# Performance work log

Hardware: AMD Instinct MI355X
Metric: run time of the kernel (lower is better)

The kernel has to match this reference:

```python
import jax, jax.numpy as jnp
import numpy as np

B, N, C, O = 8, 4096, 256, 256  # batch, nodes, in_channels, out_channels
DENSITY = 0.01


def _cheb_k2(x_flat, A, W0, W1, b):
    """PyG ChebConv with K=2, sym normalization, lambda_max=2.
    Scaled Laplacian reduces to Lhat = -D^{-1/2} A D^{-1/2} (self-loops removed,
    diagonal of I - Ahat cancels with the fill_value=-1 self loops).
    Only the first N flattened nodes have edges (faithful to the source bug)."""
    n = A.shape[0]
    A = A * (1.0 - jnp.eye(n, dtype=A.dtype))  # remove_self_loops
    deg = A.sum(axis=1)                         # scatter(edge_weight, row)
    dis = jnp.where(deg > 0, jax.lax.rsqrt(jnp.where(deg > 0, deg, 1.0)), 0.0)
    Ahat = (dis[:, None] * A) * dis[None, :]    # D^{-1/2} A D^{-1/2}
    out = x_flat @ W0                           # Tx_0 term, all B*N nodes
    prop = -(Ahat @ x_flat[:n])                 # Tx_1 = Lhat x, first N nodes only
    out = out.at[:n].add(prop @ W1)
    return out + b


def setup_inputs() -> dict:
    key = jax.random.key(0)
    ks = jax.random.split(key, 12)
    x = jax.random.normal(ks[0], (B, N, C), jnp.float32)

    def adj(k):
        u = jax.random.uniform(k, (N, N), jnp.float32)
        return jnp.where(u < DENSITY, u, 0.0)

    adj1 = adj(ks[1])
    adj2 = adj(ks[2])
    s = 0.02
    Wc0_a = jax.random.normal(ks[3], (C, O), jnp.float32) * s
    Wc1_a = jax.random.normal(ks[4], (C, O), jnp.float32) * s
    bc_a = jnp.zeros((O,), jnp.float32)
    Wc0_b = jax.random.normal(ks[5], (C, O), jnp.float32) * s
    Wc1_b = jax.random.normal(ks[6], (C, O), jnp.float32) * s
    bc_b = jnp.zeros((O,), jnp.float32)
    Wp = jax.random.normal(ks[7], (2 * O, O), jnp.float32) * s  # [in,out] layout
    bp = jnp.zeros((O,), jnp.float32)
    return {"x": x, "adj1": adj1, "adj2": adj2,
            "Wc0_a": Wc0_a, "Wc1_a": Wc1_a, "bc_a": bc_a,
            "Wc0_b": Wc0_b, "Wc1_b": Wc1_b, "bc_b": bc_b,
            "Wp": Wp, "bp": bp}


def reference(x, adj1, adj2, Wc0_a, Wc1_a, bc_a, Wc0_b, Wc1_b, bc_b, Wp, bp):
    b, n, c = x.shape
    x_flat = x.reshape(-1, c)  # [B*N, C]
    o1 = _cheb_k2(x_flat, adj1, Wc0_a, Wc1_a, bc_a).reshape(b, n, -1)
    o2 = _cheb_k2(x_flat, adj2, Wc0_b, Wc1_b, bc_b).reshape(b, n, -1)
    out = jnp.concatenate([o1, o2], axis=-1)  # [B, N, 2*O]
    out = out @ Wp + bp                        # projection (dropout p=0)
    return out
```

## Files before the change

kernel.cpp:

```cpp
#include <hip/hip_runtime.h>
#include <hip/hip_bf16.h>
#include <stdint.h>

typedef __bf16 bf16;
typedef __attribute__((ext_vector_type(8))) __bf16 bf16x8;
typedef __attribute__((ext_vector_type(4))) float f32x4;


#define RCAP 96

__global__ __launch_bounds__(256) void k_prep(const float* __restrict__ adj1,
                                              const float* __restrict__ adj2,
                                              float* __restrict__ dis,
                                              int* __restrict__ ccnt,
                                              unsigned short* __restrict__ cidx,
                                              float* __restrict__ cval) {
  int t = threadIdx.x;
  int wave = t >> 6, lane = t & 63;
  int gw = blockIdx.x * 4 + wave;
  int which = gw >> 12;
  int row = gw & 4095;
  const float* A = which ? adj2 : adj1;
  const f32x4* Arow = (const f32x4*)(A + (size_t)row * 4096);
  size_t base = (size_t)gw * RCAP;
  unsigned long long lmask = (1ULL << lane) - 1ULL;

  f32x4 vbuf[16];
#pragma unroll
  for (int it = 0; it < 16; ++it)
    vbuf[it] = __builtin_nontemporal_load(Arow + it * 64 + lane);

  float s = 0.f;
  int cnt = 0;
#pragma unroll
  for (int it = 0; it < 16; ++it) {
    f32x4 v = vbuf[it];
    int j0 = it * 256 + lane * 4;
#pragma unroll
    for (int k = 0; k < 4; ++k) {
      float f = v[k];
      int j = j0 + k;
      bool keep = (f != 0.f) && (j != row);
      if (j != row) s += f;
      unsigned long long bm = __ballot(keep);
      if (keep) {
        int pos = cnt + __popcll(bm & lmask);
        if (pos < RCAP) {
          cidx[base + pos] = (unsigned short)j;
          cval[base + pos] = f;
        }
      }
      cnt += (int)__popcll(bm);
    }
  }
#pragma unroll
  for (int off = 32; off >= 1; off >>= 1) s += __shfl_down(s, off, 64);
  if (lane == 0) {
    dis[gw] = (s > 0.f) ? (1.0f / sqrtf(s)) : 0.f;
    ccnt[gw] = (cnt > RCAP) ? RCAP : cnt;
  }
}

__global__ __launch_bounds__(256) void k_spmm2(const float* __restrict__ x,
                                               const float* __restrict__ dis,
                                               const int* __restrict__ ccnt,
                                               const unsigned short* __restrict__ cidx,
                                               const float* __restrict__ cval,
                                               bf16* __restrict__ P) {
  __shared__ float s_val[RCAP];
  __shared__ int s_idx[RCAP];
  int t = threadIdx.x;
  int row = blockIdx.x;
  int which = blockIdx.y;
  int r = (which << 12) | row;
  const float* dsel = dis + (which << 12);
  int n = ccnt[r];
  size_t base = (size_t)r * RCAP;
  if (t < n) {
    int j = cidx[base + t];
    s_idx[t] = j;
    s_val[t] = cval[base + t] * dsel[j];
  }
  __syncthreads();
  float acc = 0.f;
  int e = 0;
  for (; e + 4 <= n; e += 4) {
    float v0 = x[(size_t)s_idx[e + 0] * 256 + t];
    float v1 = x[(size_t)s_idx[e + 1] * 256 + t];
    float v2 = x[(size_t)s_idx[e + 2] * 256 + t];
    float v3 = x[(size_t)s_idx[e + 3] * 256 + t];
    acc += s_val[e + 0] * v0 + s_val[e + 1] * v1 + s_val[e + 2] * v2 + s_val[e + 3] * v3;
  }
  for (; e < n; ++e) acc += s_val[e] * x[(size_t)s_idx[e] * 256 + t];
  float prop = -dsel[row] * acc;
  P[(size_t)row * 512 + (size_t)which * 256 + t] = (bf16)prop;
}

__global__ __launch_bounds__(1024) void k_wprep(const float* __restrict__ W0a,
                                                const float* __restrict__ W1a,
                                                const float* __restrict__ bca,
                                                const float* __restrict__ W0b,
                                                const float* __restrict__ W1b,
                                                const float* __restrict__ bcb,
                                                const float* __restrict__ Wp,
                                                const float* __restrict__ bp,
                                                bf16* __restrict__ WxT,
                                                bf16* __restrict__ WextT,
                                                float* __restrict__ biasv) {
  __shared__ float red0[4][256], red1[4][256], red2[4][256], red3[4][256];
  int tid = threadIdx.x;
  int o = tid & 255;
  int ch = tid >> 8;
  int c = blockIdx.x;
  const float* r0a = W0a + (size_t)c * 256;
  const float* r0b = W0b + (size_t)c * 256;
  const float* r1a = W1a + (size_t)c * 256;
  const float* r1b = W1b + (size_t)c * 256;
  float ax = 0.f, a1 = 0.f, a2 = 0.f, bacc = 0.f;
#pragma unroll 8
  for (int mm = 0; mm < 64; ++mm) {
    int m = ch * 64 + mm;
    float wpt = Wp[(size_t)m * 256 + o];
    float wpb = Wp[(size_t)(m + 256) * 256 + o];
    float wa = r0a[m], wb = r0b[m];
    float w1 = r1a[m], w2 = r1b[m];
    ax += wa * wpt + wb * wpb;
    a1 += w1 * wpt;
    a2 += w2 * wpb;
    bacc += bca[m] * wpt + bcb[m] * wpb;
  }
  red0[ch][o] = ax; red1[ch][o] = a1; red2[ch][o] = a2; red3[ch][o] = bacc;
  __syncthreads();
  if (ch == 0) {
    ax = red0[0][o] + red0[1][o] + red0[2][o] + red0[3][o];
    a1 = red1[0][o] + red1[1][o] + red1[2][o] + red1[3][o];
    a2 = red2[0][o] + red2[1][o] + red2[2][o] + red2[3][o];
    bacc = red3[0][o] + red3[1][o] + red3[2][o] + red3[3][o];
    WxT[(size_t)o * 256 + c] = (bf16)ax;
    WextT[(size_t)o * 512 + c] = (bf16)a1;
    WextT[(size_t)o * 512 + 256 + c] = (bf16)a2;
    if (c == 0) biasv[o] = bacc + bp[o];
  }
}

__device__ __forceinline__ void mfma_tile(const char* ldsA, const char* ldsB,
                                          int wm, int wn, int lr, int quad,
                                          f32x4 acc[4][4]) {
  bf16x8 af[4], bb[4];
#pragma unroll
  for (int mf = 0; mf < 4; ++mf)
    af[mf] = *(const bf16x8*)(ldsA + ((wm * 64 + mf * 16 + lr) * 64 + quad * 16));
#pragma unroll
  for (int nf = 0; nf < 4; ++nf)
    bb[nf] = *(const bf16x8*)(ldsB + ((wn * 64 + nf * 16 + lr) * 64 + quad * 16));
#pragma unroll
  for (int mf = 0; mf < 4; ++mf)
#pragma unroll
    for (int nf = 0; nf < 4; ++nf)
      acc[mf][nf] = __builtin_amdgcn_mfma_f32_16x16x32_bf16(af[mf], bb[nf], acc[mf][nf], 0, 0, 0);
}

__global__ __launch_bounds__(256, 2) void k_gemm(const float* __restrict__ X,
                                                 const bf16* __restrict__ P,
                                                 const bf16* __restrict__ WxT,
                                                 const bf16* __restrict__ WextT,
                                                 const float* __restrict__ biasv,
                                                 float* __restrict__ out) {
  __shared__ __attribute__((aligned(16))) char ldsA[8192];
  __shared__ __attribute__((aligned(16))) char ldsB[8192];
  int t = threadIdx.x;
  int lane = t & 63, wave = t >> 6;
  int wm = wave & 1, wn = wave >> 1;
  int lr = lane & 15, quad = lane >> 4;
  int yy = blockIdx.y;
  int my = ((yy & 3) << 6) | (yy >> 2);
  int R0 = my * 128;
  int N0 = blockIdx.x * 128;

  f32x4 acc[4][4];
#pragma unroll
  for (int i = 0; i < 4; ++i)
#pragma unroll
    for (int j = 0; j < 4; ++j) acc[i][j] = (f32x4){0.f, 0.f, 0.f, 0.f};

  int srow = t >> 2;
  int scol = (t & 3) * 8;

#pragma unroll 1
  for (int step = 0; step < 8; ++step) {
    int kb = step * 32;
    const float* xp0 = X + (size_t)(R0 + srow) * 256 + kb + scol;
    const float* xp1 = X + (size_t)(R0 + srow + 64) * 256 + kb + scol;
    f32x4 f00 = *(const f32x4*)(xp0), f01 = *(const f32x4*)(xp0 + 4);
    f32x4 f10 = *(const f32x4*)(xp1), f11 = *(const f32x4*)(xp1 + 4);
    bf16x8 a0, a1;
#pragma unroll
    for (int k = 0; k < 4; ++k) {
      a0[k] = (bf16)f00[k]; a0[k + 4] = (bf16)f01[k];
      a1[k] = (bf16)f10[k]; a1[k + 4] = (bf16)f11[k];
    }
    bf16x8 b0 = *(const bf16x8*)(WxT + (size_t)(N0 + srow) * 256 + kb + scol);
    bf16x8 b1 = *(const bf16x8*)(WxT + (size_t)(N0 + srow + 64) * 256 + kb + scol);
    __syncthreads();
    *(bf16x8*)(ldsA + t * 16) = a0;
    *(bf16x8*)(ldsA + 4096 + t * 16) = a1;
    *(bf16x8*)(ldsB + t * 16) = b0;
    *(bf16x8*)(ldsB + 4096 + t * 16) = b1;
    __syncthreads();
    mfma_tile(ldsA, ldsB, wm, wn, lr, quad, acc);
  }

  if (R0 < 4096) {
#pragma unroll 1
    for (int step = 0; step < 16; ++step) {
      int kb = step * 32;
      bf16x8 a0 = *(const bf16x8*)(P + (size_t)(R0 + srow) * 512 + kb + scol);
      bf16x8 a1 = *(const bf16x8*)(P + (size_t)(R0 + srow + 64) * 512 + kb + scol);
      bf16x8 b0 = *(const bf16x8*)(WextT + (size_t)(N0 + srow) * 512 + kb + scol);
      bf16x8 b1 = *(const bf16x8*)(WextT + (size_t)(N0 + srow + 64) * 512 + kb + scol);
      __syncthreads();
      *(bf16x8*)(ldsA + t * 16) = a0;
      *(bf16x8*)(ldsA + 4096 + t * 16) = a1;
      *(bf16x8*)(ldsB + t * 16) = b0;
      *(bf16x8*)(ldsB + 4096 + t * 16) = b1;
      __syncthreads();
      mfma_tile(ldsA, ldsB, wm, wn, lr, quad, acc);
    }
  }

#pragma unroll
  for (int nf = 0; nf < 4; ++nf) {
    int ocol = N0 + wn * 64 + nf * 16 + lr;
    float bv = biasv[ocol];
#pragma unroll
    for (int mf = 0; mf < 4; ++mf) {
      int orow = R0 + wm * 64 + mf * 16 + quad * 4;
#pragma unroll
      for (int r = 0; r < 4; ++r)
        out[(size_t)(orow + r) * 256 + ocol] = acc[mf][nf][r] + bv;
    }
  }
}

extern "C" void kernel_launch(void* const* d_in, const int* in_sizes, int n_in,
                              void* d_out, int out_size, void* d_ws, size_t ws_size,
                              hipStream_t stream) {
  const float* x    = (const float*)d_in[0];
  const float* adj1 = (const float*)d_in[1];
  const float* adj2 = (const float*)d_in[2];
  const float* W0a  = (const float*)d_in[3];
  const float* W1a  = (const float*)d_in[4];
  const float* bca  = (const float*)d_in[5];
  const float* W0b  = (const float*)d_in[6];
  const float* W1b  = (const float*)d_in[7];
  const float* bcb  = (const float*)d_in[8];
  const float* Wp   = (const float*)d_in[9];
  const float* bp   = (const float*)d_in[10];
  float* out = (float*)d_out;

  char* ws = (char*)d_ws;
  float* dis   = (float*)(ws);
  float* biasv = (float*)(ws + 32 * 1024);
  bf16*  WxT   = (bf16*)(ws + 64 * 1024);
  bf16*  WextT = (bf16*)(ws + 320 * 1024);
  bf16*  P     = (bf16*)(ws + 704 * 1024);
  int*   ccnt  = (int*)(ws + 4800 * 1024);
  float* cval  = (float*)(ws + 4832 * 1024);
  unsigned short* cidx = (unsigned short*)(ws + 7904 * 1024);

  k_prep<<<dim3(2048), dim3(256), 0, stream>>>(adj1, adj2, dis, ccnt, cidx, cval);
  k_wprep<<<dim3(256), dim3(1024), 0, stream>>>(W0a, W1a, bca, W0b, W1b, bcb, Wp, bp,
                                                WxT, WextT, biasv);
  k_spmm2<<<dim3(4096, 2), dim3(256), 0, stream>>>(x, dis, ccnt, cidx, cval, P);
  k_gemm<<<dim3(2, 256), dim3(256), 0, stream>>>(x, P, WxT, WextT, biasv, out);
}
```

Baseline: 247.1 us.

## Merge weight prep into adjacency prep kernel and prefetch GEMM tiles into registers

The weight-folding work now runs in the first 256 blocks of the adjacency prep kernel instead of a separate launch, which removes one kernel launch and lets both jobs run concurrently. Each of those blocks now uses 256 threads looping over all 256 m instead of 1024 threads with an LDS reduction. The sparse aggregation loop gains an 8-way unrolled path to keep more gathers in flight. The GEMM loads the next K-slice of global data into registers before running the MFMAs on the current slice, overlapping memory latency with compute at the cost of more registers.

```diff
diff --git a/kernel.cpp b/kernel.cpp
--- a/kernel.cpp
+++ b/kernel.cpp
@@ -11,13 +11,48 @@
 
 __global__ __launch_bounds__(256) void k_prep(const float* __restrict__ adj1,
                                               const float* __restrict__ adj2,
+                                              const float* __restrict__ W0a,
+                                              const float* __restrict__ W1a,
+                                              const float* __restrict__ bca,
+                                              const float* __restrict__ W0b,
+                                              const float* __restrict__ W1b,
+                                              const float* __restrict__ bcb,
+                                              const float* __restrict__ Wp,
+                                              const float* __restrict__ bp,
                                               float* __restrict__ dis,
                                               int* __restrict__ ccnt,
                                               unsigned short* __restrict__ cidx,
-                                              float* __restrict__ cval) {
+                                              float* __restrict__ cval,
+                                              bf16* __restrict__ WxT,
+                                              bf16* __restrict__ WextT,
+                                              float* __restrict__ biasv) {
   int t = threadIdx.x;
+  if (blockIdx.x < 256) {
+    int c = blockIdx.x, o = t;
+    const float* r0a = W0a + (size_t)c * 256;
+    const float* r0b = W0b + (size_t)c * 256;
+    const float* r1a = W1a + (size_t)c * 256;
+    const float* r1b = W1b + (size_t)c * 256;
+    float ax = 0.f, a1 = 0.f, a2 = 0.f, bacc = 0.f;
+#pragma unroll 8
+    for (int m = 0; m < 256; ++m) {
+      float wpt = Wp[(size_t)m * 256 + o];
+      float wpb = Wp[(size_t)(m + 256) * 256 + o];
+      float wa = r0a[m], wb = r0b[m];
+      float w1 = r1a[m], w2 = r1b[m];
+      ax += wa * wpt + wb * wpb;
+      a1 += w1 * wpt;
+      a2 += w2 * wpb;
+      bacc += bca[m] * wpt + bcb[m] * wpb;
+    }
+    WxT[(size_t)o * 256 + c] = (bf16)ax;
+    WextT[(size_t)o * 512 + c] = (bf16)a1;
+    WextT[(size_t)o * 512 + 256 + c] = (bf16)a2;
+    if (c == 0) biasv[o] = bacc + bp[o];
+    return;
+  }
   int wave = t >> 6, lane = t & 63;
-  int gw = blockIdx.x * 4 + wave;
+  int gw = (blockIdx.x - 256) * 4 + wave;
   int which = gw >> 12;
   int row = gw & 4095;
   const float* A = which ? adj2 : adj1;
@@ -84,6 +119,18 @@
   __syncthreads();
   float acc = 0.f;
   int e = 0;
+  for (; e + 8 <= n; e += 8) {
+    float v0 = x[(size_t)s_idx[e + 0] * 256 + t];
+    float v1 = x[(size_t)s_idx[e + 1] * 256 + t];
+    float v2 = x[(size_t)s_idx[e + 2] * 256 + t];
+    float v3 = x[(size_t)s_idx[e + 3] * 256 + t];
+    float v4 = x[(size_t)s_idx[e + 4] * 256 + t];
+    float v5 = x[(size_t)s_idx[e + 5] * 256 + t];
+    float v6 = x[(size_t)s_idx[e + 6] * 256 + t];
+    float v7 = x[(size_t)s_idx[e + 7] * 256 + t];
+    acc += s_val[e + 0] * v0 + s_val[e + 1] * v1 + s_val[e + 2] * v2 + s_val[e + 3] * v3 +
+           s_val[e + 4] * v4 + s_val[e + 5] * v5 + s_val[e + 6] * v6 + s_val[e + 7] * v7;
+  }
   for (; e + 4 <= n; e += 4) {
     float v0 = x[(size_t)s_idx[e + 0] * 256 + t];
     float v1 = x[(size_t)s_idx[e + 1] * 256 + t];
@@ -94,53 +141,6 @@
   for (; e < n; ++e) acc += s_val[e] * x[(size_t)s_idx[e] * 256 + t];
   float prop = -dsel[row] * acc;
   P[(size_t)row * 512 + (size_t)which * 256 + t] = (bf16)prop;
-}
-
-__global__ __launch_bounds__(1024) void k_wprep(const float* __restrict__ W0a,
-                                                const float* __restrict__ W1a,
-                                                const float* __restrict__ bca,
-                                                const float* __restrict__ W0b,
-                                                const float* __restrict__ W1b,
-                                                const float* __restrict__ bcb,
-                                                const float* __restrict__ Wp,
-                                                const float* __restrict__ bp,
-                                                bf16* __restrict__ WxT,
-                                                bf16* __restrict__ WextT,
-                                                float* __restrict__ biasv) {
-  __shared__ float red0[4][256], red1[4][256], red2[4][256], red3[4][256];
-  int tid = threadIdx.x;
-  int o = tid & 255;
-  int ch = tid >> 8;
-  int c = blockIdx.x;
-  const float* r0a = W0a + (size_t)c * 256;
-  const float* r0b = W0b + (size_t)c * 256;
-  const float* r1a = W1a + (size_t)c * 256;
-  const float* r1b = W1b + (size_t)c * 256;
-  float ax = 0.f, a1 = 0.f, a2 = 0.f, bacc = 0.f;
-#pragma unroll 8
-  for (int mm = 0; mm < 64; ++mm) {
-    int m = ch * 64 + mm;
-    float wpt = Wp[(size_t)m * 256 + o];
-    float wpb = Wp[(size_t)(m + 256) * 256 + o];
-    float wa = r0a[m], wb = r0b[m];
-    float w1 = r1a[m], w2 = r1b[m];
-    ax += wa * wpt + wb * wpb;
-    a1 += w1 * wpt;
-    a2 += w2 * wpb;
-    bacc += bca[m] * wpt + bcb[m] * wpb;
-  }
-  red0[ch][o] = ax; red1[ch][o] = a1; red2[ch][o] = a2; red3[ch][o] = bacc;
-  __syncthreads();
-  if (ch == 0) {
-    ax = red0[0][o] + red0[1][o] + red0[2][o] + red0[3][o];
-    a1 = red1[0][o] + red1[1][o] + red1[2][o] + red1[3][o];
-    a2 = red2[0][o] + red2[1][o] + red2[2][o] + red2[3][o];
-    bacc = red3[0][o] + red3[1][o] + red3[2][o] + red3[3][o];
-    WxT[(size_t)o * 256 + c] = (bf16)ax;
-    WextT[(size_t)o * 512 + c] = (bf16)a1;
-    WextT[(size_t)o * 512 + 256 + c] = (bf16)a2;
-    if (c == 0) biasv[o] = bacc + bp[o];
-  }
 }
 
 __device__ __forceinline__ void mfma_tile(const char* ldsA, const char* ldsB,
@@ -186,44 +186,68 @@
   int srow = t >> 2;
   int scol = (t & 3) * 8;
 
+  const float* xb0 = X + (size_t)(R0 + srow) * 256 + scol;
+  const float* xb1 = X + (size_t)(R0 + srow + 64) * 256 + scol;
+  const bf16* wb0 = WxT + (size_t)(N0 + srow) * 256 + scol;
+  const bf16* wb1 = WxT + (size_t)(N0 + srow + 64) * 256 + scol;
+
+  f32x4 f00 = *(const f32x4*)(xb0);
+  f32x4 f01 = *(const f32x4*)(xb0 + 4);
+  f32x4 f10 = *(const f32x4*)(xb1);
+  f32x4 f11 = *(const f32x4*)(xb1 + 4);
+  bf16x8 b0 = *(const bf16x8*)(wb0);
+  bf16x8 b1 = *(const bf16x8*)(wb1);
+
 #pragma unroll 1
   for (int step = 0; step < 8; ++step) {
-    int kb = step * 32;
-    const float* xp0 = X + (size_t)(R0 + srow) * 256 + kb + scol;
-    const float* xp1 = X + (size_t)(R0 + srow + 64) * 256 + kb + scol;
-    f32x4 f00 = *(const f32x4*)(xp0), f01 = *(const f32x4*)(xp0 + 4);
-    f32x4 f10 = *(const f32x4*)(xp1), f11 = *(const f32x4*)(xp1 + 4);
     bf16x8 a0, a1;
 #pragma unroll
     for (int k = 0; k < 4; ++k) {
       a0[k] = (bf16)f00[k]; a0[k + 4] = (bf16)f01[k];
       a1[k] = (bf16)f10[k]; a1[k + 4] = (bf16)f11[k];
     }
-    bf16x8 b0 = *(const bf16x8*)(WxT + (size_t)(N0 + srow) * 256 + kb + scol);
-    bf16x8 b1 = *(const bf16x8*)(WxT + (size_t)(N0 + srow + 64) * 256 + kb + scol);
     __syncthreads();
     *(bf16x8*)(ldsA + t * 16) = a0;
     *(bf16x8*)(ldsA + 4096 + t * 16) = a1;
     *(bf16x8*)(ldsB + t * 16) = b0;
     *(bf16x8*)(ldsB + 4096 + t * 16) = b1;
     __syncthreads();
+    if (step < 7) {
+      int kb = (step + 1) * 32;
+      f00 = *(const f32x4*)(xb0 + kb);
+      f01 = *(const f32x4*)(xb0 + kb + 4);
+      f10 = *(const f32x4*)(xb1 + kb);
+      f11 = *(const f32x4*)(xb1 + kb + 4);
+      b0 = *(const bf16x8*)(wb0 + kb);
+      b1 = *(const bf16x8*)(wb1 + kb);
+    }
     mfma_tile(ldsA, ldsB, wm, wn, lr, quad, acc);
   }
 
   if (R0 < 4096) {
+    const bf16* pb0 = P + (size_t)(R0 + srow) * 512 + scol;
+    const bf16* pb1 = P + (size_t)(R0 + srow + 64) * 512 + scol;
+    const bf16* eb0 = WextT + (size_t)(N0 + srow) * 512 + scol;
+    const bf16* eb1 = WextT + (size_t)(N0 + srow + 64) * 512 + scol;
+    bf16x8 a0 = *(const bf16x8*)(pb0);
+    bf16x8 a1 = *(const bf16x8*)(pb1);
+    bf16x8 c0 = *(const bf16x8*)(eb0);
+    bf16x8 c1 = *(const bf16x8*)(eb1);
 #pragma unroll 1
     for (int step = 0; step < 16; ++step) {
-      int kb = step * 32;
-      bf16x8 a0 = *(const bf16x8*)(P + (size_t)(R0 + srow) * 512 + kb + scol);
-      bf16x8 a1 = *(const bf16x8*)(P + (size_t)(R0 + srow + 64) * 512 + kb + scol);
-      bf16x8 b0 = *(const bf16x8*)(WextT + (size_t)(N0 + srow) * 512 + kb + scol);
-      bf16x8 b1 = *(const bf16x8*)(WextT + (size_t)(N0 + srow + 64) * 512 + kb + scol);
       __syncthreads();
       *(bf16x8*)(ldsA + t * 16) = a0;
       *(bf16x8*)(ldsA + 4096 + t * 16) = a1;
-      *(bf16x8*)(ldsB + t * 16) = b0;
-      *(bf16x8*)(ldsB + 4096 + t * 16) = b1;
+      *(bf16x8*)(ldsB + t * 16) = c0;
+      *(bf16x8*)(ldsB + 4096 + t * 16) = c1;
       __syncthreads();
+      if (step < 15) {
+        int kb = (step + 1) * 32;
+        a0 = *(const bf16x8*)(pb0 + kb);
+        a1 = *(const bf16x8*)(pb1 + kb);
+        c0 = *(const bf16x8*)(eb0 + kb);
+        c1 = *(const bf16x8*)(eb1 + kb);
+      }
       mfma_tile(ldsA, ldsB, wm, wn, lr, quad, acc);
     }
   }
@@ -268,9 +292,9 @@
   float* cval  = (float*)(ws + 4832 * 1024);
   unsigned short* cidx = (unsigned short*)(ws + 7904 * 1024);
 
-  k_prep<<<dim3(2048), dim3(256), 0, stream>>>(adj1, adj2, dis, ccnt, cidx, cval);
-  k_wprep<<<dim3(256), dim3(1024), 0, stream>>>(W0a, W1a, bca, W0b, W1b, bcb, Wp, bp,
-                                                WxT, WextT, biasv);
+  k_prep<<<dim3(2304), dim3(256), 0, stream>>>(adj1, adj2, W0a, W1a, bca, W0b, W1b, bcb,
+                                               Wp, bp, dis, ccnt, cidx, cval,
+                                               WxT, WextT, biasv);
   k_spmm2<<<dim3(4096, 2), dim3(256), 0, stream>>>(x, dis, ccnt, cidx, cval, P);
   k_gemm<<<dim3(2, 256), dim3(256), 0, stream>>>(x, P, WxT, WextT, biasv, out);
 }
```

New measurement: 233.8 us. 1.06x faster.
